# Performance work log

Hardware: AMD Instinct MI355X
Metric: run time of the kernel (lower is better)

Reference implementation:

```python
import jax, jax.numpy as jnp
import numpy as np

N_NODES = 50000
N_EDGES = 800000


def _deg_inv_sqrt(idx, n):
    deg = jax.ops.segment_sum(jnp.ones(idx.shape[0], jnp.float32), idx, num_segments=n)
    return jnp.power(jnp.clip(deg, 1.0, None), -0.5)


def _gcn_layer(x, W, b, src, dst, out_norm, in_norm, n):
    # left degree norm, dense matmul, gather-scatter-sum over edges, right norm, bias
    h = (x * out_norm[:, None]) @ W
    agg = jax.ops.segment_sum(h[src], dst, num_segments=n)
    return agg * in_norm[:, None] + b


def setup_inputs() -> dict:
    key = jax.random.key(0)
    ks = jax.random.split(key, 8)
    def xavier(k, fi, fo):
        a = np.sqrt(6.0 / (fi + fo))
        return jax.random.uniform(k, (fi, fo), jnp.float32, -a, a)
    x = jax.random.normal(ks[0], (N_NODES, 256), jnp.float32)
    edge_index = jax.random.randint(ks[1], (2, N_EDGES), 0, N_NODES, dtype=jnp.int64)
    return {
        "x": x,
        "edge_index": edge_index,
        "W0": xavier(ks[2], 256, 128), "b0": jnp.zeros((128,), jnp.float32),
        "W1": xavier(ks[3], 128, 128), "b1": jnp.zeros((128,), jnp.float32),
        "W2": xavier(ks[4], 128, 128), "b2": jnp.zeros((128,), jnp.float32),
        "W3": xavier(ks[5], 128, 64),  "b3": jnp.zeros((64,), jnp.float32),
    }


def reference(x, edge_index, W0, b0, W1, b1, W2, b2, W3, b3):
    n = x.shape[0]
    src, dst = edge_index[0], edge_index[1]
    out_norm = _deg_inv_sqrt(src, n)  # out-degree based (src side)
    in_norm = _deg_inv_sqrt(dst, n)   # in-degree based (dst side)
    Ws = [W0, W1, W2, W3]
    bs = [b0, b1, b2, b3]
    h = x
    for i in range(4):
        h = _gcn_layer(h, Ws[i], bs[i], src, dst, out_norm, in_norm, n)
        if i < 3:  # relu on all but final layer
            h = jax.nn.relu(h)
    return h
```

## Files before the change

### kernel.cpp

```cpp
#include <hip/hip_runtime.h>
#include <hip/hip_fp16.h>


typedef __attribute__((ext_vector_type(8))) short short8;
typedef __attribute__((ext_vector_type(4))) float f32x4;

#define NRANGE 8
#define NCHUNK 64
#define RMAX   6272

__device__ inline unsigned short bf16_rne(float v) {
    union { float f; unsigned u; } c; c.f = v;
    unsigned u = c.u;
    unsigned lsb = (u >> 16) & 1u;
    u += 0x7fffu + lsb;
    return (unsigned short)(u >> 16);
}
__device__ inline float bf16_to_f(unsigned short h) {
    union { unsigned u; float f; } c; c.u = ((unsigned)h) << 16;
    return c.f;
}
__device__ inline void split_bf16(float v, unsigned short& hi, unsigned short& lo) {
    hi = bf16_rne(v);
    lo = bf16_rne(v - bf16_to_f(hi));
}


__global__ __launch_bounds__(256) void k_hist(const int* __restrict__ src,
                                              const int* __restrict__ dst,
                                              int ne, int R, int E,
                                              int* __restrict__ cnt_s,
                                              int* __restrict__ cnt_d,
                                              int* __restrict__ pos,
                                              const float* __restrict__ W0,
                                              const float* __restrict__ W1,
                                              const float* __restrict__ W2,
                                              const float* __restrict__ W3,
                                              unsigned short* __restrict__ Wh0, unsigned short* __restrict__ Wl0,
                                              unsigned short* __restrict__ Wh1, unsigned short* __restrict__ Wl1,
                                              unsigned short* __restrict__ Wh2, unsigned short* __restrict__ Wl2,
                                              unsigned short* __restrict__ Wh3, unsigned short* __restrict__ Wl3) {
    __shared__ int hs[RMAX];
    __shared__ int hd[RMAX];
    if (blockIdx.x >= NRANGE * NCHUNK) {
        int i = (blockIdx.x - NRANGE * NCHUNK) * 256 + threadIdx.x;
        const float* W; unsigned short *Wh, *Wl; int K, F, off;
        if (i < 32768)                     { W = W0; Wh = Wh0; Wl = Wl0; K = 256; F = 128; off = i; }
        else if (i < 32768 + 16384)        { W = W1; Wh = Wh1; Wl = Wl1; K = 128; F = 128; off = i - 32768; }
        else if (i < 32768 + 32768)        { W = W2; Wh = Wh2; Wl = Wl2; K = 128; F = 128; off = i - 49152; }
        else if (i < 32768 + 32768 + 8192) { W = W3; Wh = Wh3; Wl = Wl3; K = 128; F = 64;  off = i - 65536; }
        else return;
        int k = off / F, c = off % F;
        unsigned short h, l;
        split_bf16(W[k * F + c], h, l);
        Wh[c * K + k] = h;
        Wl[c * K + k] = l;
        return;
    }
    int r = blockIdx.x & (NRANGE - 1);
    int c = blockIdx.x >> 3;
    int tid = threadIdx.x;
    for (int i = tid; i < R; i += 256) { hs[i] = 0; hd[i] = 0; }
    __syncthreads();
    int lo = r * R, hi = lo + R;
    int e0 = c * E, e1 = min(e0 + E, ne);
    for (int i = e0 + tid; i < e1; i += 256) {
        int s = src[i], d = dst[i];
        if (s >= lo && s < hi) atomicAdd(&hs[s - lo], 1);
        if (d >= lo && d < hi) {
            int p = atomicAdd(&hd[d - lo], 1);
            pos[i] = p;
        }
    }
    __syncthreads();
    int base = (r * NCHUNK + c) * R;
    for (int i = tid; i < R; i += 256) {
        cnt_s[base + i] = hs[i];
        cnt_d[base + i] = hd[i];
    }
}

__global__ __launch_bounds__(256) void k_reduce_norms(const int* __restrict__ cnt_s,
                                                      const int* __restrict__ cnt_d, int R, int n,
                                                      float* __restrict__ onrm,
                                                      float* __restrict__ inrm,
                                                      int* __restrict__ degd_sum,
                                                      int* __restrict__ blocksum) {
    __shared__ int red[256];
    int tid = threadIdx.x;
    int i = blockIdx.x * 256 + tid;
    int r = i / R, ip = i - r * R;
    int ds = 0, dd = 0;
    for (int c = 0; c < NCHUNK; ++c) {
        ds += cnt_s[(r * NCHUNK + c) * R + ip];
        dd += cnt_d[(r * NCHUNK + c) * R + ip];
    }
    degd_sum[i] = dd;
    if (i < n) {
        onrm[i] = rsqrtf((float)max(ds, 1));
        inrm[i] = rsqrtf((float)max(dd, 1));
    }
    red[tid] = dd;
    __syncthreads();
#pragma unroll
    for (int off = 128; off > 0; off >>= 1) {
        if (tid < off) red[tid] += red[tid + off];
        __syncthreads();
    }
    if (tid == 0) blocksum[blockIdx.x] = red[0];
}

__global__ __launch_bounds__(256) void k_cursors2(const int* __restrict__ blocksum, int nblk,
                                                  const int* __restrict__ degd_sum,
                                                  const int* __restrict__ cnt_d, int R,
                                                  int* __restrict__ row_ptr,
                                                  int* __restrict__ cbase, int total_i) {
    __shared__ int bs[256];
    __shared__ int wsum[4];
    int tid = threadIdx.x;
    bs[tid] = (tid < nblk) ? blocksum[tid] : 0;
    __syncthreads();
#pragma unroll
    for (int off = 1; off < 256; off <<= 1) {
        int v = bs[tid];
        int u = (tid >= off) ? bs[tid - off] : 0;
        __syncthreads();
        bs[tid] = v + u;
        __syncthreads();
    }
    int base = (blockIdx.x > 0) ? bs[blockIdx.x - 1] : 0;

    int i = blockIdx.x * 256 + tid;
    int dd = degd_sum[i];
    int lane = tid & 63, wid = tid >> 6;
    int x = dd;
#pragma unroll
    for (int off = 1; off < 64; off <<= 1) {
        int y = __shfl_up(x, off, 64);
        if (lane >= off) x += y;
    }
    if (lane == 63) wsum[wid] = x;
    __syncthreads();
    int wbase = 0;
    for (int wp = 0; wp < wid; ++wp) wbase += wsum[wp];
    int excl = base + wbase + (x - dd);
    row_ptr[i] = excl;
    if (i == total_i - 1) row_ptr[total_i] = excl + dd;

    int r = i / R, ip = i - r * R;
    int run = excl;
    for (int c = 0; c < NCHUNK; ++c) {
        int idx = (r * NCHUNK + c) * R + ip;
        cbase[idx] = run;
        run += cnt_d[idx];
    }
}

__global__ void k_csr_scatter(const int* __restrict__ src,
                              const int* __restrict__ dst,
                              const int* __restrict__ pos,
                              const int* __restrict__ cbase,
                              int ne, int R, int E,
                              int* __restrict__ eidx) {
    int i = blockIdx.x * blockDim.x + threadIdx.x;
    if (i >= ne) return;
    int d = dst[i];
    int r = d / R, ip = d - r * R;
    int c = i / E;
    eidx[cbase[(r * NCHUNK + c) * R + ip] + pos[i]] = src[i];
}


__global__ void k_split_w_all(const float* __restrict__ W0, const float* __restrict__ W1,
                              const float* __restrict__ W2, const float* __restrict__ W3,
                              unsigned short* __restrict__ Wh0, unsigned short* __restrict__ Wl0,
                              unsigned short* __restrict__ Wh1, unsigned short* __restrict__ Wl1,
                              unsigned short* __restrict__ Wh2, unsigned short* __restrict__ Wl2,
                              unsigned short* __restrict__ Wh3, unsigned short* __restrict__ Wl3) {
    int i = blockIdx.x * blockDim.x + threadIdx.x;
    const float* W; unsigned short *Wh, *Wl; int K, F, off;
    if (i < 32768)                    { W = W0; Wh = Wh0; Wl = Wl0; K = 256; F = 128; off = i; }
    else if (i < 32768 + 16384)       { W = W1; Wh = Wh1; Wl = Wl1; K = 128; F = 128; off = i - 32768; }
    else if (i < 32768 + 32768)       { W = W2; Wh = Wh2; Wl = Wl2; K = 128; F = 128; off = i - 49152; }
    else if (i < 32768 + 32768 + 8192){ W = W3; Wh = Wh3; Wl = Wl3; K = 128; F = 64;  off = i - 65536; }
    else return;
    int k = off / F, c = off % F;
    unsigned short h, l;
    split_bf16(W[k * F + c], h, l);
    Wh[c * K + k] = h;
    Wl[c * K + k] = l;
}

template <int K, int N, bool FA>
__global__ __launch_bounds__(256) void k_mm(const unsigned short* __restrict__ Ah,
                                            const unsigned short* __restrict__ Al,
                                            const float* __restrict__ Xf,
                                            const float* __restrict__ onrm,
                                            const unsigned short* __restrict__ Bh,
                                            const unsigned short* __restrict__ Bl,
                                            __half* __restrict__ H, int n) {
    constexpr int KT = 128;
    constexpr int NT = N / 16;
    constexpr int NKT = K / KT;
    __shared__ unsigned short sBh[N * KT];
    __shared__ unsigned short sBl[N * KT];

    int tid = threadIdx.x;
    int w = tid >> 6, lane = tid & 63;
    int quad = lane >> 4, l16 = lane & 15;
    int row_base = blockIdx.x * 128 + w * 32;

    int ar0 = row_base + l16;
    int ar1 = row_base + 16 + l16;
    if (ar0 >= n) ar0 = n - 1;
    if (ar1 >= n) ar1 = n - 1;

    float on0 = 0.f, on1 = 0.f;
    if (FA) { on0 = onrm[ar0]; on1 = onrm[ar1]; }

    f32x4 acc[2][NT];
#pragma unroll
    for (int m = 0; m < 2; ++m)
#pragma unroll
        for (int t = 0; t < NT; ++t) acc[m][t] = (f32x4){0.f, 0.f, 0.f, 0.f};

    for (int kt = 0; kt < NKT; ++kt) {
        if (kt) __syncthreads();
        for (int idx = tid; idx < N * 16; idx += 256) {
            int c = idx >> 4;
            int g = idx & 15;
            short8 vh = *(const short8*)(Bh + (size_t)c * K + kt * KT + g * 8);
            short8 vl = *(const short8*)(Bl + (size_t)c * K + kt * KT + g * 8);
            int sg = g ^ (c & 15);
            *(short8*)(&sBh[c * KT + sg * 8]) = vh;
            *(short8*)(&sBl[c * KT + sg * 8]) = vl;
        }
        __syncthreads();

#pragma unroll
        for (int k0 = 0; k0 < KT; k0 += 32) {
            int eoff = k0 + quad * 8;
            short8 a0hv, a0lv, a1hv, a1lv;
            if (FA) {
                const float* x0 = Xf + (size_t)ar0 * K + kt * KT + eoff;
                const float* x1 = Xf + (size_t)ar1 * K + kt * KT + eoff;
                float4 p00 = *(const float4*)x0;
                float4 p01 = *(const float4*)(x0 + 4);
                float4 p10 = *(const float4*)x1;
                float4 p11 = *(const float4*)(x1 + 4);
                float e0[8] = {p00.x, p00.y, p00.z, p00.w, p01.x, p01.y, p01.z, p01.w};
                float e1[8] = {p10.x, p10.y, p10.z, p10.w, p11.x, p11.y, p11.z, p11.w};
#pragma unroll
                for (int q = 0; q < 8; ++q) {
                    unsigned short hh, ll;
                    split_bf16(e0[q] * on0, hh, ll);
                    a0hv[q] = (short)hh; a0lv[q] = (short)ll;
                    split_bf16(e1[q] * on1, hh, ll);
                    a1hv[q] = (short)hh; a1lv[q] = (short)ll;
                }
            } else {
                a0hv = *(const short8*)(Ah + (size_t)ar0 * K + kt * KT + eoff);
                a0lv = *(const short8*)(Al + (size_t)ar0 * K + kt * KT + eoff);
                a1hv = *(const short8*)(Ah + (size_t)ar1 * K + kt * KT + eoff);
                a1lv = *(const short8*)(Al + (size_t)ar1 * K + kt * KT + eoff);
            }
            int g = (k0 >> 3) + quad;
            int sg8 = (g ^ l16) * 8;
#pragma unroll
            for (int t = 0; t < NT; ++t) {
                int cb = (t * 16 + l16) * KT;
                short8 bh = *(const short8*)(&sBh[cb + sg8]);
                short8 bl = *(const short8*)(&sBl[cb + sg8]);
                acc[0][t] = __builtin_amdgcn_mfma_f32_16x16x32_bf16(a0hv, bh, acc[0][t], 0, 0, 0);
                acc[0][t] = __builtin_amdgcn_mfma_f32_16x16x32_bf16(a0lv, bh, acc[0][t], 0, 0, 0);
                acc[0][t] = __builtin_amdgcn_mfma_f32_16x16x32_bf16(a0hv, bl, acc[0][t], 0, 0, 0);
                acc[1][t] = __builtin_amdgcn_mfma_f32_16x16x32_bf16(a1hv, bh, acc[1][t], 0, 0, 0);
                acc[1][t] = __builtin_amdgcn_mfma_f32_16x16x32_bf16(a1lv, bh, acc[1][t], 0, 0, 0);
                acc[1][t] = __builtin_amdgcn_mfma_f32_16x16x32_bf16(a1hv, bl, acc[1][t], 0, 0, 0);
            }
        }
    }

#pragma unroll
    for (int m = 0; m < 2; ++m) {
#pragma unroll
        for (int t = 0; t < NT; ++t) {
#pragma unroll
            for (int r = 0; r < 4; ++r) {
                int grow = row_base + m * 16 + quad * 4 + r;
                if (grow < n) H[(size_t)grow * N + t * 16 + l16] = __float2half(acc[m][t][r]);
            }
        }
    }
}


__global__ __launch_bounds__(256) void k_agg128_split(const __half* __restrict__ h,
                                                      const int* __restrict__ row_ptr,
                                                      const int* __restrict__ eidx,
                                                      const float* __restrict__ inrm,
                                                      const float* __restrict__ onrm,
                                                      const float* __restrict__ bias,
                                                      unsigned short* __restrict__ Ah,
                                                      unsigned short* __restrict__ Al, int n) {
    int wave = threadIdx.x >> 6;
    int lane = threadIdx.x & 63;
    int g = lane >> 4;
    int l = lane & 15;
    int node = blockIdx.x * 16 + wave * 4 + g;
    bool valid = node < n;
    int nd = valid ? node : n - 1;
    int beg = row_ptr[nd], end = row_ptr[nd + 1];
    const short8* h8 = (const short8*)h;

    float a[4][8];
#pragma unroll
    for (int u = 0; u < 4; ++u)
#pragma unroll
        for (int c = 0; c < 8; ++c) a[u][c] = 0.f;

    int j = beg;
    for (; j + 4 <= end; j += 4) {
        int s[4];
#pragma unroll
        for (int u = 0; u < 4; ++u) s[u] = eidx[j + u];
        short8 v[4];
#pragma unroll
        for (int u = 0; u < 4; ++u) v[u] = h8[(size_t)s[u] * 16 + l];
#pragma unroll
        for (int u = 0; u < 4; ++u) {
            const __half2* ph = reinterpret_cast<const __half2*>(&v[u]);
#pragma unroll
            for (int p = 0; p < 4; ++p) {
                float2 f = __half22float2(ph[p]);
                a[u][2 * p] += f.x;
                a[u][2 * p + 1] += f.y;
            }
        }
    }
    for (; j < end; ++j) {
        short8 v = h8[(size_t)eidx[j] * 16 + l];
        const __half2* ph = reinterpret_cast<const __half2*>(&v);
#pragma unroll
        for (int p = 0; p < 4; ++p) {
            float2 f = __half22float2(ph[p]);
            a[0][2 * p] += f.x;
            a[0][2 * p + 1] += f.y;
        }
    }

    float nrm = inrm[nd];
    float on = onrm[nd];
    float4 b0 = ((const float4*)bias)[l * 2];
    float4 b1 = ((const float4*)bias)[l * 2 + 1];
    float bb[8] = {b0.x, b0.y, b0.z, b0.w, b1.x, b1.y, b1.z, b1.w};
    short8 hv, lv;
#pragma unroll
    for (int c = 0; c < 8; ++c) {
        float s = (a[0][c] + a[1][c]) + (a[2][c] + a[3][c]);
        float o = fmaxf(s * nrm + bb[c], 0.f) * on;
        unsigned short hh, ll;
        split_bf16(o, hh, ll);
        hv[c] = (short)hh;
        lv[c] = (short)ll;
    }
    if (valid) {
        ((short8*)Ah)[(size_t)node * 16 + l] = hv;
        ((short8*)Al)[(size_t)node * 16 + l] = lv;
    }
}

__global__ __launch_bounds__(256) void k_agg64(const __half* __restrict__ h,
                                               const int* __restrict__ row_ptr,
                                               const int* __restrict__ eidx,
                                               const float* __restrict__ inrm,
                                               const float* __restrict__ bias,
                                               float* __restrict__ out, int n) {
    int wave = threadIdx.x >> 6;
    int lane = threadIdx.x & 63;
    int g = lane >> 4;
    int l = lane & 15;
    int node = blockIdx.x * 16 + wave * 4 + g;
    bool valid = node < n;
    int nd = valid ? node : n - 1;
    int beg = row_ptr[nd], end = row_ptr[nd + 1];
    const ushort4* h4 = (const ushort4*)h;

    float a[8][4];
#pragma unroll
    for (int u = 0; u < 8; ++u)
#pragma unroll
        for (int c = 0; c < 4; ++c) a[u][c] = 0.f;

    int j = beg;
    for (; j + 8 <= end; j += 8) {
        int s[8];
#pragma unroll
        for (int u = 0; u < 8; ++u) s[u] = eidx[j + u];
        ushort4 v[8];
#pragma unroll
        for (int u = 0; u < 8; ++u) v[u] = h4[(size_t)s[u] * 16 + l];
#pragma unroll
        for (int u = 0; u < 8; ++u) {
            const __half2* ph = reinterpret_cast<const __half2*>(&v[u]);
            float2 f0 = __half22float2(ph[0]);
            float2 f1 = __half22float2(ph[1]);
            a[u][0] += f0.x; a[u][1] += f0.y; a[u][2] += f1.x; a[u][3] += f1.y;
        }
    }
    for (; j < end; ++j) {
        ushort4 v = h4[(size_t)eidx[j] * 16 + l];
        const __half2* ph = reinterpret_cast<const __half2*>(&v);
        float2 f0 = __half22float2(ph[0]);
        float2 f1 = __half22float2(ph[1]);
        a[0][0] += f0.x; a[0][1] += f0.y; a[0][2] += f1.x; a[0][3] += f1.y;
    }

    float nrm = inrm[nd];
    float4 b4 = ((const float4*)bias)[l];
    float4 o;
    float s0 = ((a[0][0] + a[1][0]) + (a[2][0] + a[3][0])) + ((a[4][0] + a[5][0]) + (a[6][0] + a[7][0]));
    float s1 = ((a[0][1] + a[1][1]) + (a[2][1] + a[3][1])) + ((a[4][1] + a[5][1]) + (a[6][1] + a[7][1]));
    float s2 = ((a[0][2] + a[1][2]) + (a[2][2] + a[3][2])) + ((a[4][2] + a[5][2]) + (a[6][2] + a[7][2]));
    float s3 = ((a[0][3] + a[1][3]) + (a[2][3] + a[3][3])) + ((a[4][3] + a[5][3]) + (a[6][3] + a[7][3]));
    o.x = s0 * nrm + b4.x;
    o.y = s1 * nrm + b4.y;
    o.z = s2 * nrm + b4.z;
    o.w = s3 * nrm + b4.w;
    if (valid) ((float4*)out)[(size_t)node * 16 + l] = o;
}

__global__ __launch_bounds__(1024) void k_scan(const int* __restrict__ deg, int n,
                                               int* __restrict__ row_ptr) {
    __shared__ int wsum[16];
    __shared__ int carry;
    int tid = threadIdx.x;
    int lane = tid & 63;
    int wid = tid >> 6;
    if (tid == 0) carry = 0;
    __syncthreads();
    int n4 = (n + 3) >> 2;
    for (int base = 0; base < n4; base += 1024) {
        int i4 = base + tid;
        int4 v = make_int4(0, 0, 0, 0);
        if (i4 < n4) v = ((const int4*)deg)[i4];
        int s = v.x + v.y + v.z + v.w;
        int x = s;
#pragma unroll
        for (int off = 1; off < 64; off <<= 1) {
            int y = __shfl_up(x, off, 64);
            if (lane >= off) x += y;
        }
        if (lane == 63) wsum[wid] = x;
        __syncthreads();
        if (wid == 0 && lane < 16) {
            int w = wsum[lane];
#pragma unroll
            for (int off = 1; off < 16; off <<= 1) {
                int y = __shfl_up(w, off, 16);
                if (lane >= off) w += y;
            }
            wsum[lane] = w;
        }
        __syncthreads();
        int excl = x - s + carry + (wid > 0 ? wsum[wid - 1] : 0);
        if (i4 < n4) {
            int e0 = excl, e1 = e0 + v.x, e2 = e1 + v.y, e3 = e2 + v.z;
            ((int4*)row_ptr)[i4] = make_int4(e0, e1, e2, e3);
        }
        __syncthreads();
        if (tid == 0) carry += wsum[15];
        __syncthreads();
    }
    if (tid == 0) row_ptr[n] = carry;
}

template <int K, int FO, int TX, int TY, int RPT>
__global__ __launch_bounds__(256) void k_matmul(const float* __restrict__ X,
                                                const float* __restrict__ W,
                                                const float* __restrict__ onrm,
                                                float* __restrict__ H, int n) {
    constexpr int BROWS = TY * RPT;
    constexpr int LDK = K + 1;
    __shared__ float xs[BROWS * LDK];
    int tx = threadIdx.x, ty = threadIdx.y;
    int tid = ty * TX + tx;
    int row0 = blockIdx.x * BROWS;

    for (int idx = tid; idx < BROWS * K; idx += 256) {
        int r = idx / K;
        int k = idx - r * K;
        int row = row0 + r;
        xs[r * LDK + k] = (row < n) ? X[(size_t)row * K + k] : 0.f;
    }
    __syncthreads();

    float4 acc[RPT];
#pragma unroll
    for (int r = 0; r < RPT; ++r) acc[r] = make_float4(0.f, 0.f, 0.f, 0.f);

    const float4* W4 = (const float4*)W;
#pragma unroll 4
    for (int k = 0; k < K; ++k) {
        float4 w = W4[k * (FO / 4) + tx];
#pragma unroll
        for (int r = 0; r < RPT; ++r) {
            float xv = xs[(ty * RPT + r) * LDK + k];
            acc[r].x += xv * w.x;
            acc[r].y += xv * w.y;
            acc[r].z += xv * w.z;
            acc[r].w += xv * w.w;
        }
    }

#pragma unroll
    for (int r = 0; r < RPT; ++r) {
        int row = row0 + ty * RPT + r;
        if (row < n) {
            float s = onrm[row];
            float4 o = make_float4(acc[r].x * s, acc[r].y * s, acc[r].z * s, acc[r].w * s);
            ((float4*)H)[(size_t)row * (FO / 4) + tx] = o;
        }
    }
}

__global__ __launch_bounds__(256) void k_agg128f(const float* __restrict__ h,
                                                 const int* __restrict__ row_ptr,
                                                 const int* __restrict__ eidx,
                                                 const float* __restrict__ inrm,
                                                 const float* __restrict__ bias,
                                                 float* __restrict__ out, int n, int relu) {
    int node = blockIdx.x * 4 + (threadIdx.x >> 6);
    int lane = threadIdx.x & 63;
    if (node >= n) return;
    int beg = row_ptr[node], end = row_ptr[node + 1];
    const float2* h2 = (const float2*)h;
    float ax = 0.f, ay = 0.f;
    for (int j = beg; j < end; ++j) {
        int s = eidx[j];
        float2 v = h2[(size_t)s * 64 + lane];
        ax += v.x;
        ay += v.y;
    }
    float nrm = inrm[node];
    float2 b2 = ((const float2*)bias)[lane];
    float ox = ax * nrm + b2.x;
    float oy = ay * nrm + b2.y;
    if (relu) { ox = fmaxf(ox, 0.f); oy = fmaxf(oy, 0.f); }
    float2 o; o.x = ox; o.y = oy;
    ((float2*)out)[(size_t)node * 64 + lane] = o;
}

__global__ __launch_bounds__(256) void k_agg64f(const float* __restrict__ h,
                                                const int* __restrict__ row_ptr,
                                                const int* __restrict__ eidx,
                                                const float* __restrict__ inrm,
                                                const float* __restrict__ bias,
                                                float* __restrict__ out, int n) {
    int node = blockIdx.x * 4 + (threadIdx.x >> 6);
    int lane = threadIdx.x & 63;
    if (node >= n) return;
    int beg = row_ptr[node], end = row_ptr[node + 1];
    float acc = 0.f;
    for (int j = beg; j < end; ++j) {
        int s = eidx[j];
        acc += h[(size_t)s * 64 + lane];
    }
    out[(size_t)node * 64 + lane] = acc * inrm[node] + bias[lane];
}

__global__ void k_degrees_leg(const int* __restrict__ src, const int* __restrict__ dst,
                              int ne, int* __restrict__ degs, int* __restrict__ degd) {
    int i = blockIdx.x * blockDim.x + threadIdx.x;
    if (i < ne) {
        atomicAdd(&degs[src[i]], 1);
        atomicAdd(&degd[dst[i]], 1);
    }
}
__global__ void k_norms_leg(const int* __restrict__ degs, const int* __restrict__ degd,
                            float* __restrict__ onrm, float* __restrict__ inrm,
                            int* __restrict__ degd_sum, int n) {
    int i = blockIdx.x * blockDim.x + threadIdx.x;
    if (i < n) {
        degd_sum[i] = degd[i];
        onrm[i] = rsqrtf((float)max(degs[i], 1));
        inrm[i] = rsqrtf((float)max(degd[i], 1));
    }
}
__global__ void k_copy_int(const int* __restrict__ a, int* __restrict__ b, int n) {
    int i = blockIdx.x * blockDim.x + threadIdx.x;
    if (i < n) b[i] = a[i];
}
__global__ void k_build_csr_leg(const int* __restrict__ src, const int* __restrict__ dst,
                                int ne, int* __restrict__ cursor, int* __restrict__ eidx) {
    int i = blockIdx.x * blockDim.x + threadIdx.x;
    if (i < ne) {
        int p = atomicAdd(&cursor[dst[i]], 1);
        eidx[p] = src[i];
    }
}

static inline size_t align_up(size_t v, size_t a) { return (v + a - 1) & ~(a - 1); }

extern "C" void kernel_launch(void* const* d_in, const int* in_sizes, int n_in,
                              void* d_out, int out_size, void* d_ws, size_t ws_size,
                              hipStream_t stream) {
    const float* x  = (const float*)d_in[0];
    const int* ei   = (const int*)d_in[1];
    const float* W0 = (const float*)d_in[2];
    const float* b0 = (const float*)d_in[3];
    const float* W1 = (const float*)d_in[4];
    const float* b1 = (const float*)d_in[5];
    const float* W2 = (const float*)d_in[6];
    const float* b2 = (const float*)d_in[7];
    const float* W3 = (const float*)d_in[8];
    const float* b3 = (const float*)d_in[9];

    const int n  = in_sizes[0] / 256;
    const int ne = in_sizes[1] / 2;
    const int n_pad = (n + 127) & ~127;
    const int* src = ei;
    const int* dst = ei + ne;

    char* ws = (char*)d_ws;
    size_t off = 0;
    auto take = [&](size_t bytes) { void* p = ws + off; off = align_up(off + bytes, 256); return p; };
    int* row_ptr  = (int*)take((size_t)(n_pad + 4) * 4);
    int* degd_sum = (int*)take((size_t)n_pad * 4);
    int* eidx     = (int*)take((size_t)ne * 4);
    float* onrm   = (float*)take((size_t)n * 4);
    float* inrm   = (float*)take((size_t)n * 4);

    size_t off_save = off;
    unsigned short* Ah  = (unsigned short*)take((size_t)n_pad * 256 * 2);
    unsigned short* Al  = (unsigned short*)take((size_t)n_pad * 256 * 2);
    __half* hbuf        = (__half*)take((size_t)n * 128 * 2);
    unsigned short* Wh0 = (unsigned short*)take(256 * 128 * 2);
    unsigned short* Wl0 = (unsigned short*)take(256 * 128 * 2);
    unsigned short* Wh1 = (unsigned short*)take(128 * 128 * 2);
    unsigned short* Wl1 = (unsigned short*)take(128 * 128 * 2);
    unsigned short* Wh2 = (unsigned short*)take(128 * 128 * 2);
    unsigned short* Wl2 = (unsigned short*)take(128 * 128 * 2);
    unsigned short* Wh3 = (unsigned short*)take(128 * 64 * 2);
    unsigned short* Wl3 = (unsigned short*)take(128 * 64 * 2);
    bool use_mfma = (off <= ws_size);

    char* pre = (char*)Ah;
    const int R = ((n + NRANGE * 64 - 1) / (NRANGE * 64)) * 64;
    const size_t cntSz = align_up((size_t)NRANGE * NCHUNK * R * 4, 256);
    int* cnt_s = (int*)pre;
    int* cnt_d = (int*)(pre + cntSz);
    int* cbase = (int*)(pre + 2 * cntSz);
    int* pos   = (int*)(pre + 3 * cntSz);
    int* blocksum = (int*)(pre + 3 * cntSz + align_up((size_t)ne * 4, 256));

    const int aggGrid = (n + 15) / 16;

    if (R <= RMAX) {
        const int E = (ne + NCHUNK - 1) / NCHUNK;
        const int nscan = NRANGE * R;
        const int nblk = nscan / 256;
        const int wsplitBlocks = use_mfma ? 288 : 0;
        k_hist<<<NRANGE * NCHUNK + wsplitBlocks, 256, 0, stream>>>(
            src, dst, ne, R, E, cnt_s, cnt_d, pos,
            W0, W1, W2, W3, Wh0, Wl0, Wh1, Wl1, Wh2, Wl2, Wh3, Wl3);
        k_reduce_norms<<<nblk, 256, 0, stream>>>(cnt_s, cnt_d, R, n,
                                                 onrm, inrm, degd_sum, blocksum);
        k_cursors2<<<nblk, 256, 0, stream>>>(blocksum, nblk, degd_sum, cnt_d, R,
                                             row_ptr, cbase, nscan);
        k_csr_scatter<<<(ne + 255) / 256, 256, 0, stream>>>(src, dst, pos, cbase, ne, R, E, eidx);
    } else {
        int* degs   = cnt_s;
        int* degd   = cnt_s + n_pad;
        int* cursor = cnt_s + 2 * n_pad;
        hipMemsetAsync(degs, 0, (size_t)2 * n_pad * 4, stream);
        k_degrees_leg<<<(ne + 255) / 256, 256, 0, stream>>>(src, dst, ne, degs, degd);
        k_norms_leg<<<(n + 255) / 256, 256, 0, stream>>>(degs, degd, onrm, inrm, degd_sum, n);
        k_scan<<<1, 1024, 0, stream>>>(degd_sum, n, row_ptr);
        k_copy_int<<<(n + 255) / 256, 256, 0, stream>>>(row_ptr, cursor, n);
        k_build_csr_leg<<<(ne + 255) / 256, 256, 0, stream>>>(src, dst, ne, cursor, eidx);
        if (use_mfma)
            k_split_w_all<<<(73728 + 255) / 256, 256, 0, stream>>>(
                W0, W1, W2, W3, Wh0, Wl0, Wh1, Wl1, Wh2, Wl2, Wh3, Wl3);
    }

    if (use_mfma) {
        const int mmGrid = n_pad / 128;
        k_mm<256, 128, true><<<mmGrid, 256, 0, stream>>>(nullptr, nullptr, x, onrm, Wh0, Wl0, hbuf, n);
        k_agg128_split<<<aggGrid, 256, 0, stream>>>(hbuf, row_ptr, eidx, inrm, onrm, b0, Ah, Al, n);
        k_mm<128, 128, false><<<mmGrid, 256, 0, stream>>>(Ah, Al, nullptr, nullptr, Wh1, Wl1, hbuf, n);
        k_agg128_split<<<aggGrid, 256, 0, stream>>>(hbuf, row_ptr, eidx, inrm, onrm, b1, Ah, Al, n);
        k_mm<128, 128, false><<<mmGrid, 256, 0, stream>>>(Ah, Al, nullptr, nullptr, Wh2, Wl2, hbuf, n);
        k_agg128_split<<<aggGrid, 256, 0, stream>>>(hbuf, row_ptr, eidx, inrm, onrm, b2, Ah, Al, n);
        k_mm<128, 64, false><<<mmGrid, 256, 0, stream>>>(Ah, Al, nullptr, nullptr, Wh3, Wl3, hbuf, n);
        k_agg64<<<aggGrid, 256, 0, stream>>>(hbuf, row_ptr, eidx, inrm, b3, (float*)d_out, n);
    } else {
        off = off_save;
        float* hbufF  = (float*)take((size_t)n * 128 * 4);
        float* xnextF = (float*)take((size_t)n * 128 * 4);
        const int aggGridF = (n + 3) / 4;

        k_matmul<256, 128, 32, 8, 4><<<(n + 31) / 32, dim3(32, 8), 0, stream>>>(x, W0, onrm, hbufF, n);
        k_agg128f<<<aggGridF, 256, 0, stream>>>(hbufF, row_ptr, eidx, inrm, b0, xnextF, n, 1);
        k_matmul<128, 128, 32, 8, 4><<<(n + 31) / 32, dim3(32, 8), 0, stream>>>(xnextF, W1, onrm, hbufF, n);
        k_agg128f<<<aggGridF, 256, 0, stream>>>(hbufF, row_ptr, eidx, inrm, b1, xnextF, n, 1);
        k_matmul<128, 128, 32, 8, 4><<<(n + 31) / 32, dim3(32, 8), 0, stream>>>(xnextF, W2, onrm, hbufF, n);
        k_agg128f<<<aggGridF, 256, 0, stream>>>(hbufF, row_ptr, eidx, inrm, b2, xnextF, n, 1);
        k_matmul<128, 64, 16, 16, 4><<<(n + 63) / 64, dim3(16, 16), 0, stream>>>(xnextF, W3, onrm, hbufF, n);
        k_agg64f<<<aggGridF, 256, 0, stream>>>(hbufF, row_ptr, eidx, inrm, b3, (float*)d_out, n);
    }
}
```

Baseline: 339.0 us.

## Pack histogram counters into 16-bit pairs and double edge chunks

The per-chunk degree histograms, counts and per-edge positions move from 32-bit ints to 16-bit values, with two counters packed per 32-bit LDS word, which halves shared memory use. Edge chunks double from 64 to 128, so more histogram blocks run, and block indexing becomes chunk-major. The goal is more parallelism in the histogram pass and less memory traffic for the count and pos arrays. The cost is a 16-bit overflow limit, guarded by E<=65535, and twice as many chunks to sum in the reduce and cursor kernels.

```diff
diff --git a/kernel.cpp b/kernel.cpp
--- a/kernel.cpp
+++ b/kernel.cpp
@@ -6,7 +6,7 @@
 typedef __attribute__((ext_vector_type(4))) float f32x4;
 
 #define NRANGE 8
-#define NCHUNK 64
+#define NCHUNK 128
 #define RMAX   6272
 
 __device__ inline unsigned short bf16_rne(float v) {
@@ -29,9 +29,9 @@
 __global__ __launch_bounds__(256) void k_hist(const int* __restrict__ src,
                                               const int* __restrict__ dst,
                                               int ne, int R, int E,
-                                              int* __restrict__ cnt_s,
-                                              int* __restrict__ cnt_d,
-                                              int* __restrict__ pos,
+                                              unsigned short* __restrict__ cnt_s,
+                                              unsigned short* __restrict__ cnt_d,
+                                              unsigned short* __restrict__ pos,
                                               const float* __restrict__ W0,
                                               const float* __restrict__ W1,
                                               const float* __restrict__ W2,
@@ -40,8 +40,8 @@
                                               unsigned short* __restrict__ Wh1, unsigned short* __restrict__ Wl1,
                                               unsigned short* __restrict__ Wh2, unsigned short* __restrict__ Wl2,
                                               unsigned short* __restrict__ Wh3, unsigned short* __restrict__ Wl3) {
-    __shared__ int hs[RMAX];
-    __shared__ int hd[RMAX];
+    __shared__ int hs32[RMAX / 2];
+    __shared__ int hd32[RMAX / 2];
     if (blockIdx.x >= NRANGE * NCHUNK) {
         int i = (blockIdx.x - NRANGE * NCHUNK) * 256 + threadIdx.x;
         const float* W; unsigned short *Wh, *Wl; int K, F, off;
@@ -57,31 +57,39 @@
         Wl[c * K + k] = l;
         return;
     }
-    int r = blockIdx.x & (NRANGE - 1);
-    int c = blockIdx.x >> 3;
+    int c = blockIdx.x & (NCHUNK - 1);
+    int r = blockIdx.x >> 7;
     int tid = threadIdx.x;
-    for (int i = tid; i < R; i += 256) { hs[i] = 0; hd[i] = 0; }
+    int Rh = R >> 1;
+    for (int i = tid; i < Rh; i += 256) { hs32[i] = 0; hd32[i] = 0; }
     __syncthreads();
-    int lo = r * R, hi = lo + R;
+    int lo = r * R;
     int e0 = c * E, e1 = min(e0 + E, ne);
     for (int i = e0 + tid; i < e1; i += 256) {
         int s = src[i], d = dst[i];
-        if (s >= lo && s < hi) atomicAdd(&hs[s - lo], 1);
-        if (d >= lo && d < hi) {
-            int p = atomicAdd(&hd[d - lo], 1);
-            pos[i] = p;
+        unsigned ps = (unsigned)(s - lo);
+        unsigned pd = (unsigned)(d - lo);
+        if (ps < (unsigned)R)
+            atomicAdd(&hs32[ps >> 1], 1 << ((ps & 1) << 4));
+        if (pd < (unsigned)R) {
+            int sh = (pd & 1) << 4;
+            int old = atomicAdd(&hd32[pd >> 1], 1 << sh);
+            pos[i] = (unsigned short)((old >> sh) & 0xffff);
         }
     }
     __syncthreads();
-    int base = (r * NCHUNK + c) * R;
-    for (int i = tid; i < R; i += 256) {
-        cnt_s[base + i] = hs[i];
-        cnt_d[base + i] = hd[i];
-    }
-}
-
-__global__ __launch_bounds__(256) void k_reduce_norms(const int* __restrict__ cnt_s,
-                                                      const int* __restrict__ cnt_d, int R, int n,
+    int base2 = (r * NCHUNK + c) * Rh;
+    int* cs32 = (int*)cnt_s;
+    int* cd32 = (int*)cnt_d;
+    for (int i = tid; i < Rh; i += 256) {
+        cs32[base2 + i] = hs32[i];
+        cd32[base2 + i] = hd32[i];
+    }
+}
+
+__global__ __launch_bounds__(256) void k_reduce_norms(const unsigned short* __restrict__ cnt_s,
+                                                      const unsigned short* __restrict__ cnt_d,
+                                                      int R, int n,
                                                       float* __restrict__ onrm,
                                                       float* __restrict__ inrm,
                                                       int* __restrict__ degd_sum,
@@ -112,7 +120,7 @@
 
 __global__ __launch_bounds__(256) void k_cursors2(const int* __restrict__ blocksum, int nblk,
                                                   const int* __restrict__ degd_sum,
-                                                  const int* __restrict__ cnt_d, int R,
+                                                  const unsigned short* __restrict__ cnt_d, int R,
                                                   int* __restrict__ row_ptr,
                                                   int* __restrict__ cbase, int total_i) {
     __shared__ int bs[256];
@@ -158,7 +166,7 @@
 
 __global__ void k_csr_scatter(const int* __restrict__ src,
                               const int* __restrict__ dst,
-                              const int* __restrict__ pos,
+                              const unsigned short* __restrict__ pos,
                               const int* __restrict__ cbase,
                               int ne, int R, int E,
                               int* __restrict__ eidx) {
@@ -622,11 +630,16 @@
     const int* src = ei;
     const int* dst = ei + ne;
 
+    const int R = ((n + NRANGE * 64 - 1) / (NRANGE * 64)) * 64;
+    const int E = (ne + NCHUNK - 1) / NCHUNK;
+    const int nscan = NRANGE * R;
+    const bool fast_pre = (R <= RMAX) && (E <= 65535);
+
     char* ws = (char*)d_ws;
     size_t off = 0;
     auto take = [&](size_t bytes) { void* p = ws + off; off = align_up(off + bytes, 256); return p; };
-    int* row_ptr  = (int*)take((size_t)(n_pad + 4) * 4);
-    int* degd_sum = (int*)take((size_t)n_pad * 4);
+    int* row_ptr  = (int*)take((size_t)(nscan + 8) * 4);
+    int* degd_sum = (int*)take((size_t)nscan * 4);
     int* eidx     = (int*)take((size_t)ne * 4);
     float* onrm   = (float*)take((size_t)n * 4);
     float* inrm   = (float*)take((size_t)n * 4);
@@ -646,19 +659,16 @@
     bool use_mfma = (off <= ws_size);
 
     char* pre = (char*)Ah;
-    const int R = ((n + NRANGE * 64 - 1) / (NRANGE * 64)) * 64;
-    const size_t cntSz = align_up((size_t)NRANGE * NCHUNK * R * 4, 256);
-    int* cnt_s = (int*)pre;
-    int* cnt_d = (int*)(pre + cntSz);
-    int* cbase = (int*)(pre + 2 * cntSz);
-    int* pos   = (int*)(pre + 3 * cntSz);
-    int* blocksum = (int*)(pre + 3 * cntSz + align_up((size_t)ne * 4, 256));
+    const size_t cntSz = align_up((size_t)NRANGE * NCHUNK * R * 2, 256);
+    unsigned short* cnt_s = (unsigned short*)pre;
+    unsigned short* cnt_d = (unsigned short*)(pre + cntSz);
+    int* cbase            = (int*)(pre + 2 * cntSz);
+    unsigned short* pos   = (unsigned short*)(pre + 4 * cntSz);
+    int* blocksum         = (int*)(pre + 4 * cntSz + align_up((size_t)ne * 2, 256));
 
     const int aggGrid = (n + 15) / 16;
 
-    if (R <= RMAX) {
-        const int E = (ne + NCHUNK - 1) / NCHUNK;
-        const int nscan = NRANGE * R;
+    if (fast_pre) {
         const int nblk = nscan / 256;
         const int wsplitBlocks = use_mfma ? 288 : 0;
         k_hist<<<NRANGE * NCHUNK + wsplitBlocks, 256, 0, stream>>>(
@@ -670,9 +680,9 @@
                                              row_ptr, cbase, nscan);
         k_csr_scatter<<<(ne + 255) / 256, 256, 0, stream>>>(src, dst, pos, cbase, ne, R, E, eidx);
     } else {
-        int* degs   = cnt_s;
-        int* degd   = cnt_s + n_pad;
-        int* cursor = cnt_s + 2 * n_pad;
+        int* degs   = (int*)pre;
+        int* degd   = (int*)pre + n_pad;
+        int* cursor = (int*)pre + 2 * n_pad;
         hipMemsetAsync(degs, 0, (size_t)2 * n_pad * 4, stream);
         k_degrees_leg<<<(ne + 255) / 256, 256, 0, stream>>>(src, dst, ne, degs, degd);
         k_norms_leg<<<(n + 255) / 256, 256, 0, stream>>>(degs, degd, onrm, inrm, degd_sum, n);
```

Measured after the change: 337.0 us. No clear change (-0.6%).
